# Optimization experiments

Measured on AMD Instinct MI355X. Metric: run time of the kernel, lower is better.

Reference implementation:

```python
import jax, jax.numpy as jnp
import numpy as np

N = 20000
E = 400000
D = 128  # latent_dim


def _bce(p, t):
    # torch F.binary_cross_entropy clamps log terms at -100
    logp = jnp.clip(jnp.log(p), -100.0)
    log1mp = jnp.clip(jnp.log(1.0 - p), -100.0)
    return -jnp.mean(t * logp + (1.0 - t) * log1mp)


def setup_inputs() -> dict:
    key = jax.random.key(0)
    ks = jax.random.split(key, 12)
    pos = jax.random.normal(ks[0], (N,), jnp.float32)
    s = jax.random.uniform(ks[1], (N,), dtype=jnp.float32)
    edge_index = jax.random.randint(ks[2], (2, E), 0, N)
    pi = jax.random.randint(ks[3], (E,), 0, 2)
    pi_h = jax.random.randint(ks[4], (4, E), 0, 2)
    reach_h = jax.random.randint(ks[5], (4, N), 0, 2)
    sc = 0.1
    W_enc = sc * jax.random.normal(ks[6], (2, D), jnp.float32)
    b_enc = jnp.zeros((D,), jnp.float32)
    W_msg = sc * jax.random.normal(ks[7], (2 * D, D), jnp.float32)
    b_msg = jnp.zeros((D,), jnp.float32)
    W_self = sc * jax.random.normal(ks[8], (2 * D, D), jnp.float32)
    W_agg = sc * jax.random.normal(ks[9], (D, D), jnp.float32)
    b_upd = jnp.zeros((D,), jnp.float32)
    W_dec = sc * jax.random.normal(ks[10], (2 * D, 1), jnp.float32)
    b_dec = jnp.zeros((1,), jnp.float32)
    return dict(pos=pos, s=s, edge_index=edge_index, pi=pi, pi_h=pi_h, reach_h=reach_h,
                W_enc=W_enc, b_enc=b_enc, W_msg=W_msg, b_msg=b_msg,
                W_self=W_self, W_agg=W_agg, b_upd=b_upd, W_dec=W_dec, b_dec=b_dec)


def reference(pos, s, edge_index, pi, pi_h, reach_h,
              W_enc, b_enc, W_msg, b_msg, W_self, W_agg, b_upd, W_dec, b_dec):
    n = pos.shape[0]
    src, dst = edge_index[0], edge_index[1]
    idx_both = jnp.concatenate([src, dst])  # incident-edge readout indices
    hints = pi_h[1:].astype(jnp.float32)              # [T, E]
    hints_reach = reach_h[1:].astype(jnp.float32)     # [T, N]
    max_iter = hints.shape[0] + 1

    h = jnp.zeros((n, D), jnp.float32)
    sfeat = s
    preds, preds_y = [], []
    for _ in range(max_iter):  # small fixed iteration count (algorithm steps)
        inp = jnp.stack([pos, sfeat], axis=1)                      # [N, 2]
        z = jax.nn.relu(inp @ W_enc + b_enc)                       # encoder
        x = jnp.concatenate([z, h], axis=1)                        # [N, 2D]
        msg = jax.nn.relu(x[src] @ W_msg + b_msg)                  # [E, D]
        agg = jax.ops.segment_max(msg, dst, num_segments=n)        # scatter-max
        agg = jnp.where(jnp.isfinite(agg), agg, 0.0)
        h = jax.nn.relu(x @ W_self + agg @ W_agg + b_upd)          # processor
        ef = jnp.concatenate([h[src], h[dst]], axis=1)             # [E, 2D]
        alpha = jax.nn.sigmoid(ef @ W_dec + b_dec)[:, 0]           # decoder -> per-edge prob
        preds.append(alpha)
        # per-node max over all incident edges (both endpoints), threshold 0.8
        amax = jax.ops.segment_max(jnp.concatenate([alpha, alpha]), idx_both, num_segments=n)
        y = (amax >= 0.8).astype(jnp.float32)
        preds_y.append(y)
        sfeat = y

    predictions = jnp.stack(preds)        # [max_iter, E]
    predictions_y = jnp.stack(preds_y)    # [max_iter, N]

    loss_x = _bce(predictions[-1], pi.astype(jnp.float32))
    loss_h = jnp.asarray(0.0, jnp.float32)
    for i in range(hints.shape[0]):
        loss_h = loss_h + _bce(predictions[i], hints[i])
    y_loss_x = _bce(predictions_y[-1], reach_h[-1].astype(jnp.float32))
    y_loss_h = jnp.asarray(0.0, jnp.float32)
    for i in range(hints_reach.shape[0]):
        y_loss_h = y_loss_h + _bce(predictions_y[i], hints_reach[i])
    return (y, loss_x, loss_h, y_loss_x, y_loss_h)
```

## Files before the change

### kernel.cpp

```cpp
#include <hip/hip_runtime.h>

#define CSR_B 64

__global__ __launch_bounds__(256) void k_hist2(const int* __restrict__ eidx, int E, int N,
                                               int* __restrict__ partial_d,
                                               int* __restrict__ partial_s) {
  extern __shared__ unsigned int hist[];
  int nw = (N + 1) >> 1;
  for (int i = threadIdx.x; i < 2 * nw; i += blockDim.x) hist[i] = 0u;
  __syncthreads();
  const int* src = eidx;
  const int* dst = eidx + E;
  int chunk = (E + CSR_B - 1) / CSR_B;
  int beg = blockIdx.x * chunk, end = min(E, beg + chunk);
  for (int e = beg + threadIdx.x; e < end; e += blockDim.x) {
    int d = dst[e];
    atomicAdd(&hist[d >> 1], 1u << ((d & 1) * 16));
    int s = src[e];
    atomicAdd(&hist[nw + (s >> 1)], 1u << ((s & 1) * 16));
  }
  __syncthreads();
  for (int i = threadIdx.x; i < N; i += blockDim.x) {
    partial_d[(size_t)blockIdx.x * N + i] = (int)((hist[i >> 1] >> ((i & 1) * 16)) & 0xFFFFu);
    partial_s[(size_t)blockIdx.x * N + i] = (int)((hist[nw + (i >> 1)] >> ((i & 1) * 16)) & 0xFFFFu);
  }
}

__global__ __launch_bounds__(256) void k_colscan2(int* __restrict__ partial_d,
                                                  int* __restrict__ cnt_d,
                                                  int* __restrict__ partial_s,
                                                  int* __restrict__ cnt_s, int N) {
  int g = blockIdx.x * blockDim.x + threadIdx.x;
  int* partial;
  int* cnt;
  int bin;
  if (g < N) { partial = partial_d; cnt = cnt_d; bin = g; }
  else if (g < 2 * N) { partial = partial_s; cnt = cnt_s; bin = g - N; }
  else return;
  int run = 0;
  for (int b = 0; b < CSR_B; ++b) {
    int t = partial[(size_t)b * N + bin];
    partial[(size_t)b * N + bin] = run;
    run += t;
  }
  cnt[bin] = run;
}

__device__ __forceinline__ void scan_one(const int* __restrict__ cnt, int* __restrict__ rp,
                                         int N, int* sums) {
  int t = threadIdx.x;
  int chunk = (N + 1023) / 1024;
  int beg = t * chunk, end = min(N, beg + chunk);
  int s = 0;
  for (int i = beg; i < end; ++i) s += cnt[i];
  sums[t] = s;
  __syncthreads();
  for (int off = 1; off < 1024; off <<= 1) {
    int v = (t >= off) ? sums[t - off] : 0;
    __syncthreads();
    sums[t] += v;
    __syncthreads();
  }
  int run = (t > 0) ? sums[t - 1] : 0;
  if (t == 0) rp[0] = 0;
  for (int i = beg; i < end; ++i) { run += cnt[i]; rp[i + 1] = run; }
}

__global__ __launch_bounds__(1024) void k_scan2both(const int* __restrict__ cnt_d,
                                                    int* __restrict__ rp_d,
                                                    const int* __restrict__ cnt_s,
                                                    int* __restrict__ rp_s, int N) {
  __shared__ int sums[1024];
  scan_one(cnt_d, rp_d, N, sums);
  __syncthreads();
  scan_one(cnt_s, rp_s, N, sums);
}

__global__ __launch_bounds__(256) void k_scatter2(
    const int* __restrict__ eidx, int E, int N,
    const int* __restrict__ partial_d, const int* __restrict__ rp_d, int* __restrict__ csr_src,
    const int* __restrict__ partial_s, const int* __restrict__ rp_s, int* __restrict__ csr_dst) {
  extern __shared__ unsigned int cur[];
  int nw = (N + 1) >> 1;
  for (int i = threadIdx.x; i < 2 * nw; i += blockDim.x) cur[i] = 0u;
  __syncthreads();
  const int* src = eidx;
  const int* dst = eidx + E;
  int chunk = (E + CSR_B - 1) / CSR_B;
  int beg = blockIdx.x * chunk, end = min(E, beg + chunk);
  for (int e = beg + threadIdx.x; e < end; e += blockDim.x) {
    int d = dst[e], s = src[e];
    int shd = (d & 1) * 16;
    unsigned int old = atomicAdd(&cur[d >> 1], 1u << shd);
    csr_src[rp_d[d] + partial_d[(size_t)blockIdx.x * N + d] + (int)((old >> shd) & 0xFFFFu)] = s;
    int shs = (s & 1) * 16;
    unsigned int old2 = atomicAdd(&cur[nw + (s >> 1)], 1u << shs);
    csr_dst[rp_s[s] + partial_s[(size_t)blockIdx.x * N + s] + (int)((old2 >> shs) & 0xFFFFu)] = d;
  }
}

__global__ void k_build_w(const float* __restrict__ W_msg, const float* __restrict__ W_self,
                          const float* __restrict__ b_msg, float* __restrict__ Wcat,
                          float* __restrict__ bcat) {
  int idx = blockIdx.x * blockDim.x + threadIdx.x;
  int k = idx >> 8, j = idx & 255;
  Wcat[idx] = (j < 128) ? W_msg[k * 128 + j] : W_self[k * 128 + (j - 128)];
  if (idx < 256) bcat[idx] = (idx < 128) ? b_msg[idx] : 0.0f;
}

template <bool IT0>
__global__ __launch_bounds__(256) void k_gemm(
    const float* __restrict__ pos, const float* __restrict__ sfeat,
    const float* __restrict__ hsrc, const float* __restrict__ W_enc,
    const float* __restrict__ b_enc, const float* __restrict__ B,
    const float* __restrict__ bias, float* __restrict__ C, int M) {
  const int NC = 256;
  __shared__ float As[16][132];
  __shared__ float Bs[16][64];
  const int m0 = blockIdx.x * 128, n0 = blockIdx.y * 64;
  const int t = threadIdx.x;
  const int ty = t >> 4, tx = t & 15;
  const int lr0 = t >> 2;
  const int lq = (t & 3) << 2;
  const int r0 = m0 + lr0, r1 = r0 + 64;
  const bool v0 = r0 < M, v1 = r1 < M;
  float p0 = 0.f, s0 = 0.f, p1 = 0.f, s1 = 0.f;
  if (v0) { p0 = pos[r0]; s0 = sfeat[r0]; }
  if (v1) { p1 = pos[r1]; s1 = sfeat[r1]; }
  const int bk = t >> 4, bc = (t & 15) << 2;
  float acc[8][4] = {};
  for (int k0 = 0; k0 < 256; k0 += 16) {
    const int col = k0 + lq;
    float4 we0, we1, be;
    if (col < 128) {
      we0 = *reinterpret_cast<const float4*>(&W_enc[col]);
      we1 = *reinterpret_cast<const float4*>(&W_enc[128 + col]);
      be = *reinterpret_cast<const float4*>(&b_enc[col]);
    }
#pragma unroll
    for (int pass = 0; pass < 2; ++pass) {
      const int lr = lr0 + pass * 64;
      const int r = pass ? r1 : r0;
      const bool vv = pass ? v1 : v0;
      float4 av = make_float4(0.f, 0.f, 0.f, 0.f);
      if (vv) {
        if (col < 128) {
          const float pp = pass ? p1 : p0, ss = pass ? s1 : s0;
          av.x = fmaxf(fmaf(pp, we0.x, fmaf(ss, we1.x, be.x)), 0.f);
          av.y = fmaxf(fmaf(pp, we0.y, fmaf(ss, we1.y, be.y)), 0.f);
          av.z = fmaxf(fmaf(pp, we0.z, fmaf(ss, we1.z, be.z)), 0.f);
          av.w = fmaxf(fmaf(pp, we0.w, fmaf(ss, we1.w, be.w)), 0.f);
        } else if (!IT0) {
          av = *reinterpret_cast<const float4*>(&hsrc[(size_t)r * 128 + (col - 128)]);
        }
      }
      As[lq + 0][lr] = av.x;
      As[lq + 1][lr] = av.y;
      As[lq + 2][lr] = av.z;
      As[lq + 3][lr] = av.w;
    }
    *reinterpret_cast<float4*>(&Bs[bk][bc]) =
        *reinterpret_cast<const float4*>(&B[(size_t)(k0 + bk) * NC + n0 + bc]);
    __syncthreads();
#pragma unroll
    for (int k = 0; k < 16; ++k) {
      float4 a0 = *reinterpret_cast<const float4*>(&As[k][ty * 8]);
      float4 a1 = *reinterpret_cast<const float4*>(&As[k][ty * 8 + 4]);
      float4 b = *reinterpret_cast<const float4*>(&Bs[k][tx * 4]);
      const float a[8] = {a0.x, a0.y, a0.z, a0.w, a1.x, a1.y, a1.z, a1.w};
      const float bb[4] = {b.x, b.y, b.z, b.w};
#pragma unroll
      for (int i = 0; i < 8; ++i)
#pragma unroll
        for (int j = 0; j < 4; ++j) acc[i][j] = fmaf(a[i], bb[j], acc[i][j]);
    }
    __syncthreads();
  }
  float4 b4 = *reinterpret_cast<const float4*>(&bias[n0 + tx * 4]);
#pragma unroll
  for (int i = 0; i < 8; ++i) {
    int row = m0 + ty * 8 + i;
    if (row < M) {
      float4 o = make_float4(acc[i][0] + b4.x, acc[i][1] + b4.y, acc[i][2] + b4.z,
                             acc[i][3] + b4.w);
      *reinterpret_cast<float4*>(&C[(size_t)row * NC + n0 + tx * 4]) = o;
    }
  }
}

__device__ __forceinline__ float4 fmax4(float4 a, float4 b) {
  return make_float4(fmaxf(a.x, b.x), fmaxf(a.y, b.y), fmaxf(a.z, b.z), fmaxf(a.w, b.w));
}

__global__ __launch_bounds__(256) void k_aggmax(
    const float* __restrict__ xw, const int* __restrict__ row_ptr,
    const int* __restrict__ csr_src, float* __restrict__ agg, int N) {
  int gid = blockIdx.x * blockDim.x + threadIdx.x;
  int node = gid >> 6;
  if (node >= N) return;
  int lane = gid & 63;
  int half = lane >> 5, sub = lane & 31;
  const float* base = xw + sub * 4;
  float4 a0 = make_float4(0.f, 0.f, 0.f, 0.f);
  float4 a1 = a0, a2 = a0, a3 = a0;
  const int beg = row_ptr[node], end = row_ptr[node + 1];
  int i = beg + half;
  for (; i + 6 < end; i += 8) {
    int s0 = csr_src[i], s1 = csr_src[i + 2], s2 = csr_src[i + 4], s3 = csr_src[i + 6];
    float4 m0 = *reinterpret_cast<const float4*>(base + (size_t)s0 * 256);
    float4 m1 = *reinterpret_cast<const float4*>(base + (size_t)s1 * 256);
    float4 m2 = *reinterpret_cast<const float4*>(base + (size_t)s2 * 256);
    float4 m3 = *reinterpret_cast<const float4*>(base + (size_t)s3 * 256);
    a0 = fmax4(a0, m0);
    a1 = fmax4(a1, m1);
    a2 = fmax4(a2, m2);
    a3 = fmax4(a3, m3);
  }
  for (; i < end; i += 2) {
    int s0 = csr_src[i];
    a0 = fmax4(a0, *reinterpret_cast<const float4*>(base + (size_t)s0 * 256));
  }
  a0 = fmax4(fmax4(a0, a1), fmax4(a2, a3));
  a0.x = fmaxf(a0.x, __shfl_xor(a0.x, 32));
  a0.y = fmaxf(a0.y, __shfl_xor(a0.y, 32));
  a0.z = fmaxf(a0.z, __shfl_xor(a0.z, 32));
  a0.w = fmaxf(a0.w, __shfl_xor(a0.w, 32));
  if (half == 0) *reinterpret_cast<float4*>(&agg[(size_t)node * 128 + sub * 4]) = a0;
}

__global__ __launch_bounds__(256) void k_update2(
    const float* __restrict__ agg, const float* __restrict__ W_agg,
    const float* __restrict__ b_upd, const float* __restrict__ xw,
    const float* __restrict__ W_dec, const float* __restrict__ b_dec,
    float* __restrict__ h, float* __restrict__ u, float* __restrict__ v, int M) {
  __shared__ float As[32][33];
  __shared__ float Bs[32][128];
  const int m0 = blockIdx.x * 32;
  const int t = threadIdx.x;
  const int ty = t >> 5, tx = t & 31;
  const int lar = t >> 3, lac = (t & 7) << 2;
  float acc[4][4] = {};
  for (int k0 = 0; k0 < 128; k0 += 32) {
    {
      float4 av = make_float4(0.f, 0.f, 0.f, 0.f);
      int row = m0 + lar;
      if (row < M) av = *reinterpret_cast<const float4*>(&agg[(size_t)row * 128 + k0 + lac]);
      As[lar][lac + 0] = av.x;
      As[lar][lac + 1] = av.y;
      As[lar][lac + 2] = av.z;
      As[lar][lac + 3] = av.w;
#pragma unroll
      for (int p = 0; p < 4; ++p) {
        int br = (t >> 5) + p * 8;
        *reinterpret_cast<float4*>(&Bs[br][tx * 4]) =
            *reinterpret_cast<const float4*>(&W_agg[(size_t)(k0 + br) * 128 + tx * 4]);
      }
    }
    __syncthreads();
#pragma unroll
    for (int k = 0; k < 32; ++k) {
      float4 b4 = *reinterpret_cast<const float4*>(&Bs[k][tx * 4]);
      const float bb[4] = {b4.x, b4.y, b4.z, b4.w};
#pragma unroll
      for (int j = 0; j < 4; ++j) {
        float a = As[ty * 4 + j][k];
#pragma unroll
        for (int c = 0; c < 4; ++c) acc[j][c] = fmaf(a, bb[c], acc[j][c]);
      }
    }
    __syncthreads();
  }
  const float4 bu4 = *reinterpret_cast<const float4*>(&b_upd[tx * 4]);
  const float4 wdu = *reinterpret_cast<const float4*>(&W_dec[tx * 4]);
  const float4 wdv = *reinterpret_cast<const float4*>(&W_dec[128 + tx * 4]);
  const float bd = b_dec[0];
#pragma unroll
  for (int j = 0; j < 4; ++j) {
    int row = m0 + ty * 4 + j;
    if (row >= M) continue;
    float4 sf = *reinterpret_cast<const float4*>(&xw[(size_t)row * 256 + 128 + tx * 4]);
    float4 h4;
    h4.x = fmaxf(acc[j][0] + sf.x + bu4.x, 0.f);
    h4.y = fmaxf(acc[j][1] + sf.y + bu4.y, 0.f);
    h4.z = fmaxf(acc[j][2] + sf.z + bu4.z, 0.f);
    h4.w = fmaxf(acc[j][3] + sf.w + bu4.w, 0.f);
    *reinterpret_cast<float4*>(&h[(size_t)row * 128 + tx * 4]) = h4;
    float up = h4.x * wdu.x + h4.y * wdu.y + h4.z * wdu.z + h4.w * wdu.w;
    float vp = h4.x * wdv.x + h4.y * wdv.y + h4.z * wdv.z + h4.w * wdv.w;
#pragma unroll
    for (int m = 16; m > 0; m >>= 1) {
      up += __shfl_xor(up, m);
      vp += __shfl_xor(vp, m);
    }
    if (tx == 0) {
      u[row] = up + bd;
      v[row] = vp;
    }
  }
}

#define GB 512
__global__ __launch_bounds__(256) void k_losses(
    const int* __restrict__ src, const int* __restrict__ dst, const float* __restrict__ u,
    const float* __restrict__ v, const int* __restrict__ tgt, const int* __restrict__ row_ptr,
    const int* __restrict__ csr_src, const int* __restrict__ row_ptr2,
    const int* __restrict__ csr_dst, const int* __restrict__ reach_row,
    float* __restrict__ ybuf, float* __restrict__ yout, int write_out,
    double* __restrict__ pe_slot, double* __restrict__ py_slot, int E, int N) {
  __shared__ double wsum[4];
  double term = 0.0;
  for (int e = blockIdx.x * blockDim.x + threadIdx.x; e < E; e += GB * 256) {
    float l = u[src[e]] + v[dst[e]];
    float a = 1.0f / (1.0f + expf(-l));
    float t = (float)tgt[e];
    float lp = fmaxf(logf(a), -100.0f);
    float l1 = fmaxf(logf(1.0f - a), -100.0f);
    term += (double)(t * lp + (1.0f - t) * l1);
  }
#pragma unroll
  for (int off = 32; off > 0; off >>= 1) term += __shfl_down(term, off);
  if ((threadIdx.x & 63) == 0) wsum[threadIdx.x >> 6] = term;
  __syncthreads();
  if (threadIdx.x == 0) pe_slot[blockIdx.x] = wsum[0] + wsum[1] + wsum[2] + wsum[3];
  __syncthreads();
  double c = 0.0;
  for (int n = blockIdx.x * blockDim.x + threadIdx.x; n < N; n += GB * 256) {
    float mu = -INFINITY, mv = -INFINITY;
    const int b1 = row_ptr[n], e1 = row_ptr[n + 1];
    for (int i = b1; i < e1; ++i) mu = fmaxf(mu, u[csr_src[i]]);
    const int b2 = row_ptr2[n], e2 = row_ptr2[n + 1];
    for (int i = b2; i < e2; ++i) mv = fmaxf(mv, v[csr_dst[i]]);
    float m = fmaxf(mu + v[n], u[n] + mv);
    float a = 1.0f / (1.0f + expf(-m));
    float yv = (a >= 0.8f) ? 1.0f : 0.0f;
    ybuf[n] = yv;
    if (write_out) yout[n] = yv;
    if ((float)reach_row[n] != yv) c = 100.0;
  }
#pragma unroll
  for (int off = 32; off > 0; off >>= 1) c += __shfl_down(c, off);
  if ((threadIdx.x & 63) == 0) wsum[threadIdx.x >> 6] = c;
  __syncthreads();
  if (threadIdx.x == 0) py_slot[blockIdx.x] = wsum[0] + wsum[1] + wsum[2] + wsum[3];
}

__global__ void k_final(const double* __restrict__ pe, const double* __restrict__ py,
                        float* __restrict__ out4, int N, int E, int T) {
  __shared__ double le[8], ly[8];
  int lane = threadIdx.x;
  for (int it = 0; it < T; ++it) {
    double s = 0.0;
    for (int i = lane; i < GB; i += 64) s += pe[(size_t)it * GB + i];
#pragma unroll
    for (int off = 32; off > 0; off >>= 1) s += __shfl_down(s, off);
    if (lane == 0) le[it] = s;
    double s2 = 0.0;
    for (int i = lane; i < GB; i += 64) s2 += py[(size_t)it * GB + i];
#pragma unroll
    for (int off = 32; off > 0; off >>= 1) s2 += __shfl_down(s2, off);
    if (lane == 0) ly[it] = s2;
  }
  __syncthreads();
  if (lane == 0) {
    float loss_x = (float)(-le[T - 1] / (double)E);
    float loss_h = 0.0f;
    for (int i = 0; i < T - 1; ++i) loss_h += (float)(-le[i] / (double)E);
    float yl_x = (float)(ly[T - 1] / (double)N);
    float yl_h = 0.0f;
    for (int i = 0; i < T - 1; ++i) yl_h += (float)(ly[i] / (double)N);
    out4[0] = loss_x;
    out4[1] = loss_h;
    out4[2] = yl_x;
    out4[3] = yl_h;
  }
}

extern "C" void kernel_launch(void* const* d_in, const int* in_sizes, int n_in,
                              void* d_out, int out_size, void* d_ws, size_t ws_size,
                              hipStream_t stream) {
  const float* pos = (const float*)d_in[0];
  const float* s = (const float*)d_in[1];
  const int* eidx = (const int*)d_in[2];
  const int* pi = (const int*)d_in[3];
  const int* pi_h = (const int*)d_in[4];
  const int* reach = (const int*)d_in[5];
  const float* W_enc = (const float*)d_in[6];
  const float* b_enc = (const float*)d_in[7];
  const float* W_msg = (const float*)d_in[8];
  const float* b_msg = (const float*)d_in[9];
  const float* W_self = (const float*)d_in[10];
  const float* W_agg = (const float*)d_in[11];
  const float* b_upd = (const float*)d_in[12];
  const float* W_dec = (const float*)d_in[13];
  const float* b_dec = (const float*)d_in[14];

  const int N = in_sizes[0];
  const int E = in_sizes[3];
  const int T = in_sizes[4] / in_sizes[3];
  const int* src = eidx;
  const int* dst = eidx + E;

  char* w = (char*)d_ws;
  auto alloc = [&](size_t bytes) {
    char* p = w;
    w += (bytes + 255) & ~(size_t)255;
    return p;
  };
  float* xw = (float*)alloc((size_t)N * 256 * 4);
  float* agg = (float*)alloc((size_t)N * 128 * 4);
  float* h = (float*)alloc((size_t)N * 128 * 4);
  float* Wcat = (float*)alloc(256 * 256 * 4);
  float* bcat = (float*)alloc(256 * 4);
  float* u = (float*)alloc((size_t)N * 4);
  float* v = (float*)alloc((size_t)N * 4);
  float* ybuf = (float*)alloc((size_t)N * 4);
  int* cnt_d = (int*)alloc((size_t)N * 4);
  int* cnt_s = (int*)alloc((size_t)N * 4);
  int* row_ptr = (int*)alloc((size_t)(N + 1) * 4);
  int* row_ptr2 = (int*)alloc((size_t)(N + 1) * 4);
  int* csr_src = (int*)alloc((size_t)E * 4);
  int* csr_dst = (int*)alloc((size_t)E * 4);
  int* partial_d = (int*)alloc((size_t)CSR_B * N * 4);
  int* partial_s = (int*)alloc((size_t)CSR_B * N * 4);
  double* pe = (double*)alloc((size_t)T * GB * 8);
  double* py = (double*)alloc((size_t)T * GB * 8);

  float* outy = (float*)d_out;
  float* out4 = outy + N;

  k_build_w<<<256, 256, 0, stream>>>(W_msg, W_self, b_msg, Wcat, bcat);

  const size_t lds2 = (size_t)2 * ((N + 1) >> 1) * 4;
  k_hist2<<<CSR_B, 256, lds2, stream>>>(eidx, E, N, partial_d, partial_s);
  k_colscan2<<<(2 * N + 255) / 256, 256, 0, stream>>>(partial_d, cnt_d, partial_s, cnt_s, N);
  k_scan2both<<<1, 1024, 0, stream>>>(cnt_d, row_ptr, cnt_s, row_ptr2, N);
  k_scatter2<<<CSR_B, 256, lds2, stream>>>(eidx, E, N, partial_d, row_ptr, csr_src, partial_s,
                                           row_ptr2, csr_dst);

  const float* sfeat = s;
  for (int it = 0; it < T; ++it) {
    dim3 g1((N + 127) / 128, 4);
    if (it == 0)
      k_gemm<true><<<g1, 256, 0, stream>>>(pos, sfeat, h, W_enc, b_enc, Wcat, bcat, xw, N);
    else
      k_gemm<false><<<g1, 256, 0, stream>>>(pos, sfeat, h, W_enc, b_enc, Wcat, bcat, xw, N);

    k_aggmax<<<(N * 64 + 255) / 256, 256, 0, stream>>>(xw, row_ptr, csr_src, agg, N);

    k_update2<<<(N + 31) / 32, 256, 0, stream>>>(agg, W_agg, b_upd, xw, W_dec, b_dec,
                                                 h, u, v, N);

    const int* tgt = (it < T - 1) ? (pi_h + (size_t)(it + 1) * E) : pi;
    const int* rrow = (it < T - 1) ? (reach + (size_t)(it + 1) * N) : (reach + (size_t)(T - 1) * N);
    k_losses<<<GB, 256, 0, stream>>>(src, dst, u, v, tgt, row_ptr, csr_src, row_ptr2, csr_dst,
                                     rrow, ybuf, outy, (it == T - 1) ? 1 : 0,
                                     pe + (size_t)it * GB, py + (size_t)it * GB, E, N);
    sfeat = ybuf;
  }
  k_final<<<1, 64, 0, stream>>>(pe, py, out4, N, E, T);
}
```

Baseline: 565.8 us.

## Double-buffer GEMM tiles, restructure max-aggregation mapping, and double CSR build blocks

The fused encoder+message GEMM now uses double-buffered shared-memory tiles, so the next K-slice's global loads are issued before the current slice is computed, with one barrier per iteration instead of two. The max-aggregation kernel moves from one 64-lane wavefront per node with float4 gathers to a 2D grid where each 32-lane half-wave handles one 32-column chunk of one node with scalar loads. That grid orders the 4 column chunks and 2 node halves so that blocks running together touch nearby feature columns. CSR_B doubles to 128 to add parallelism to the histogram and scatter build, which costs more partial-count memory and scan work.

```diff
diff --git a/kernel.cpp b/kernel.cpp
--- a/kernel.cpp
+++ b/kernel.cpp
@@ -1,6 +1,6 @@
 #include <hip/hip_runtime.h>
 
-#define CSR_B 64
+#define CSR_B 128
 
 __global__ __launch_bounds__(256) void k_hist2(const int* __restrict__ eidx, int E, int N,
                                                int* __restrict__ partial_d,
@@ -108,15 +108,23 @@
   if (idx < 256) bcat[idx] = (idx < 128) ? b_msg[idx] : 0.0f;
 }
 
+__device__ __forceinline__ float4 enc4(float p, float sf, float4 we0, float4 we1, float4 be) {
+  float4 r;
+  r.x = fmaxf(fmaf(p, we0.x, fmaf(sf, we1.x, be.x)), 0.f);
+  r.y = fmaxf(fmaf(p, we0.y, fmaf(sf, we1.y, be.y)), 0.f);
+  r.z = fmaxf(fmaf(p, we0.z, fmaf(sf, we1.z, be.z)), 0.f);
+  r.w = fmaxf(fmaf(p, we0.w, fmaf(sf, we1.w, be.w)), 0.f);
+  return r;
+}
+
 template <bool IT0>
 __global__ __launch_bounds__(256) void k_gemm(
     const float* __restrict__ pos, const float* __restrict__ sfeat,
     const float* __restrict__ hsrc, const float* __restrict__ W_enc,
     const float* __restrict__ b_enc, const float* __restrict__ B,
     const float* __restrict__ bias, float* __restrict__ C, int M) {
-  const int NC = 256;
-  __shared__ float As[16][132];
-  __shared__ float Bs[16][64];
+  __shared__ float As[2][16][132];
+  __shared__ float Bs[2][16][64];
   const int m0 = blockIdx.x * 128, n0 = blockIdx.y * 64;
   const int t = threadIdx.x;
   const int ty = t >> 4, tx = t & 15;
@@ -128,51 +136,70 @@
   if (v0) { p0 = pos[r0]; s0 = sfeat[r0]; }
   if (v1) { p1 = pos[r1]; s1 = sfeat[r1]; }
   const int bk = t >> 4, bc = (t & 15) << 2;
+
+  float4 we0, we1, be, h0v, h1v, bv;
+  h0v = h1v = make_float4(0.f, 0.f, 0.f, 0.f);
+  we0 = *reinterpret_cast<const float4*>(&W_enc[lq]);
+  we1 = *reinterpret_cast<const float4*>(&W_enc[128 + lq]);
+  be  = *reinterpret_cast<const float4*>(&b_enc[lq]);
+  bv  = *reinterpret_cast<const float4*>(&B[(size_t)bk * 256 + n0 + bc]);
+  {
+    float4 a0 = make_float4(0.f, 0.f, 0.f, 0.f), a1 = a0;
+    if (v0) a0 = enc4(p0, s0, we0, we1, be);
+    if (v1) a1 = enc4(p1, s1, we0, we1, be);
+    As[0][lq + 0][lr0] = a0.x; As[0][lq + 1][lr0] = a0.y;
+    As[0][lq + 2][lr0] = a0.z; As[0][lq + 3][lr0] = a0.w;
+    As[0][lq + 0][lr0 + 64] = a1.x; As[0][lq + 1][lr0 + 64] = a1.y;
+    As[0][lq + 2][lr0 + 64] = a1.z; As[0][lq + 3][lr0 + 64] = a1.w;
+    *reinterpret_cast<float4*>(&Bs[0][bk][bc]) = bv;
+  }
+  __syncthreads();
+
   float acc[8][4] = {};
   for (int k0 = 0; k0 < 256; k0 += 16) {
-    const int col = k0 + lq;
-    float4 we0, we1, be;
-    if (col < 128) {
-      we0 = *reinterpret_cast<const float4*>(&W_enc[col]);
-      we1 = *reinterpret_cast<const float4*>(&W_enc[128 + col]);
-      be = *reinterpret_cast<const float4*>(&b_enc[col]);
-    }
-#pragma unroll
-    for (int pass = 0; pass < 2; ++pass) {
-      const int lr = lr0 + pass * 64;
-      const int r = pass ? r1 : r0;
-      const bool vv = pass ? v1 : v0;
-      float4 av = make_float4(0.f, 0.f, 0.f, 0.f);
-      if (vv) {
-        if (col < 128) {
-          const float pp = pass ? p1 : p0, ss = pass ? s1 : s0;
-          av.x = fmaxf(fmaf(pp, we0.x, fmaf(ss, we1.x, be.x)), 0.f);
-          av.y = fmaxf(fmaf(pp, we0.y, fmaf(ss, we1.y, be.y)), 0.f);
-          av.z = fmaxf(fmaf(pp, we0.z, fmaf(ss, we1.z, be.z)), 0.f);
-          av.w = fmaxf(fmaf(pp, we0.w, fmaf(ss, we1.w, be.w)), 0.f);
-        } else if (!IT0) {
-          av = *reinterpret_cast<const float4*>(&hsrc[(size_t)r * 128 + (col - 128)]);
-        }
+    const int cur = (k0 >> 4) & 1;
+    const bool more = (k0 + 16) < 256;
+    bool encn = false;
+    if (more) {
+      const int col = k0 + 16 + lq;
+      encn = col < 128;
+      if (encn) {
+        we0 = *reinterpret_cast<const float4*>(&W_enc[col]);
+        we1 = *reinterpret_cast<const float4*>(&W_enc[128 + col]);
+        be  = *reinterpret_cast<const float4*>(&b_enc[col]);
+      } else if (!IT0) {
+        if (v0) h0v = *reinterpret_cast<const float4*>(&hsrc[(size_t)r0 * 128 + col - 128]);
+        if (v1) h1v = *reinterpret_cast<const float4*>(&hsrc[(size_t)r1 * 128 + col - 128]);
       }
-      As[lq + 0][lr] = av.x;
-      As[lq + 1][lr] = av.y;
-      As[lq + 2][lr] = av.z;
-      As[lq + 3][lr] = av.w;
-    }
-    *reinterpret_cast<float4*>(&Bs[bk][bc]) =
-        *reinterpret_cast<const float4*>(&B[(size_t)(k0 + bk) * NC + n0 + bc]);
-    __syncthreads();
+      bv = *reinterpret_cast<const float4*>(&B[(size_t)(k0 + 16 + bk) * 256 + n0 + bc]);
+    }
 #pragma unroll
     for (int k = 0; k < 16; ++k) {
-      float4 a0 = *reinterpret_cast<const float4*>(&As[k][ty * 8]);
-      float4 a1 = *reinterpret_cast<const float4*>(&As[k][ty * 8 + 4]);
-      float4 b = *reinterpret_cast<const float4*>(&Bs[k][tx * 4]);
+      float4 a0 = *reinterpret_cast<const float4*>(&As[cur][k][ty * 8]);
+      float4 a1 = *reinterpret_cast<const float4*>(&As[cur][k][ty * 8 + 4]);
+      float4 b4 = *reinterpret_cast<const float4*>(&Bs[cur][k][tx * 4]);
       const float a[8] = {a0.x, a0.y, a0.z, a0.w, a1.x, a1.y, a1.z, a1.w};
-      const float bb[4] = {b.x, b.y, b.z, b.w};
+      const float bb[4] = {b4.x, b4.y, b4.z, b4.w};
 #pragma unroll
       for (int i = 0; i < 8; ++i)
 #pragma unroll
         for (int j = 0; j < 4; ++j) acc[i][j] = fmaf(a[i], bb[j], acc[i][j]);
+    }
+    if (more) {
+      float4 a0 = make_float4(0.f, 0.f, 0.f, 0.f), a1 = a0;
+      if (encn) {
+        if (v0) a0 = enc4(p0, s0, we0, we1, be);
+        if (v1) a1 = enc4(p1, s1, we0, we1, be);
+      } else if (!IT0) {
+        a0 = h0v;
+        a1 = h1v;
+      }
+      const int nxt = cur ^ 1;
+      As[nxt][lq + 0][lr0] = a0.x; As[nxt][lq + 1][lr0] = a0.y;
+      As[nxt][lq + 2][lr0] = a0.z; As[nxt][lq + 3][lr0] = a0.w;
+      As[nxt][lq + 0][lr0 + 64] = a1.x; As[nxt][lq + 1][lr0 + 64] = a1.y;
+      As[nxt][lq + 2][lr0 + 64] = a1.z; As[nxt][lq + 3][lr0 + 64] = a1.w;
+      *reinterpret_cast<float4*>(&Bs[nxt][bk][bc]) = bv;
     }
     __syncthreads();
   }
@@ -183,49 +210,38 @@
     if (row < M) {
       float4 o = make_float4(acc[i][0] + b4.x, acc[i][1] + b4.y, acc[i][2] + b4.z,
                              acc[i][3] + b4.w);
-      *reinterpret_cast<float4*>(&C[(size_t)row * NC + n0 + tx * 4]) = o;
-    }
-  }
-}
-
-__device__ __forceinline__ float4 fmax4(float4 a, float4 b) {
-  return make_float4(fmaxf(a.x, b.x), fmaxf(a.y, b.y), fmaxf(a.z, b.z), fmaxf(a.w, b.w));
+      *reinterpret_cast<float4*>(&C[(size_t)row * 256 + n0 + tx * 4]) = o;
+    }
+  }
 }
 
 __global__ __launch_bounds__(256) void k_aggmax(
     const float* __restrict__ xw, const int* __restrict__ row_ptr,
-    const int* __restrict__ csr_src, float* __restrict__ agg, int N) {
-  int gid = blockIdx.x * blockDim.x + threadIdx.x;
-  int node = gid >> 6;
-  if (node >= N) return;
-  int lane = gid & 63;
-  int half = lane >> 5, sub = lane & 31;
-  const float* base = xw + sub * 4;
-  float4 a0 = make_float4(0.f, 0.f, 0.f, 0.f);
-  float4 a1 = a0, a2 = a0, a3 = a0;
+    const int* __restrict__ csr_src, float* __restrict__ agg, int N, int Nh) {
+  const int cx = blockIdx.x & 7;
+  const int chunk = cx & 3;
+  const int half = cx >> 2;
+  const int hw = threadIdx.x >> 5;
+  const int sub = threadIdx.x & 31;
+  const int node = half * Nh + blockIdx.y * 8 + hw;
+  const int hi = half ? N : Nh;
+  if (node >= hi) return;
+  const float* base = xw + chunk * 32 + sub;
   const int beg = row_ptr[node], end = row_ptr[node + 1];
-  int i = beg + half;
-  for (; i + 6 < end; i += 8) {
-    int s0 = csr_src[i], s1 = csr_src[i + 2], s2 = csr_src[i + 4], s3 = csr_src[i + 6];
-    float4 m0 = *reinterpret_cast<const float4*>(base + (size_t)s0 * 256);
-    float4 m1 = *reinterpret_cast<const float4*>(base + (size_t)s1 * 256);
-    float4 m2 = *reinterpret_cast<const float4*>(base + (size_t)s2 * 256);
-    float4 m3 = *reinterpret_cast<const float4*>(base + (size_t)s3 * 256);
-    a0 = fmax4(a0, m0);
-    a1 = fmax4(a1, m1);
-    a2 = fmax4(a2, m2);
-    a3 = fmax4(a3, m3);
-  }
-  for (; i < end; i += 2) {
-    int s0 = csr_src[i];
-    a0 = fmax4(a0, *reinterpret_cast<const float4*>(base + (size_t)s0 * 256));
-  }
-  a0 = fmax4(fmax4(a0, a1), fmax4(a2, a3));
-  a0.x = fmaxf(a0.x, __shfl_xor(a0.x, 32));
-  a0.y = fmaxf(a0.y, __shfl_xor(a0.y, 32));
-  a0.z = fmaxf(a0.z, __shfl_xor(a0.z, 32));
-  a0.w = fmaxf(a0.w, __shfl_xor(a0.w, 32));
-  if (half == 0) *reinterpret_cast<float4*>(&agg[(size_t)node * 128 + sub * 4]) = a0;
+  float m0 = 0.f, m1 = 0.f, m2 = 0.f, m3 = 0.f;
+  int i = beg;
+  for (; i + 3 < end; i += 4) {
+    int e0 = csr_src[i], e1 = csr_src[i + 1], e2 = csr_src[i + 2], e3 = csr_src[i + 3];
+    float f0 = base[(size_t)e0 * 256];
+    float f1 = base[(size_t)e1 * 256];
+    float f2 = base[(size_t)e2 * 256];
+    float f3 = base[(size_t)e3 * 256];
+    m0 = fmaxf(m0, f0); m1 = fmaxf(m1, f1);
+    m2 = fmaxf(m2, f2); m3 = fmaxf(m3, f3);
+  }
+  for (; i < end; ++i) m0 = fmaxf(m0, base[(size_t)csr_src[i] * 256]);
+  m0 = fmaxf(fmaxf(m0, m1), fmaxf(m2, m3));
+  agg[(size_t)node * 128 + chunk * 32 + sub] = m0;
 }
 
 __global__ __launch_bounds__(256) void k_update2(
@@ -437,6 +453,9 @@
   k_scatter2<<<CSR_B, 256, lds2, stream>>>(eidx, E, N, partial_d, row_ptr, csr_src, partial_s,
                                            row_ptr2, csr_dst);
 
+  const int Nh = (N + 1) / 2;
+  const int NB = (Nh + 7) / 8;
+
   const float* sfeat = s;
   for (int it = 0; it < T; ++it) {
     dim3 g1((N + 127) / 128, 4);
@@ -445,7 +464,7 @@
     else
       k_gemm<false><<<g1, 256, 0, stream>>>(pos, sfeat, h, W_enc, b_enc, Wcat, bcat, xw, N);
 
-    k_aggmax<<<(N * 64 + 255) / 256, 256, 0, stream>>>(xw, row_ptr, csr_src, agg, N);
+    k_aggmax<<<dim3(8, NB), 256, 0, stream>>>(xw, row_ptr, csr_src, agg, N, Nh);
 
     k_update2<<<(N + 31) / 32, 256, 0, stream>>>(agg, W_agg, b_upd, xw, W_dec, b_dec,
                                                  h, u, v, N);
```

Measured after the change: 671.5 us. 1.19x slower.
